# Kernel optimization log

Hardware: AMD Instinct MI355X
Metric: run time of the kernel (lower is better)

Reference implementation:

```python
import jax, jax.numpy as jnp
import numpy as np

B, N, E, I, H = 8, 20000, 320000, 32, 64


def setup_inputs() -> dict:
    key = jax.random.key(0)
    ks = jax.random.split(key, 12)
    s = 0.05
    return {
        "x": jax.random.normal(ks[0], (B, I), jnp.float32),
        "h_prev": jax.random.normal(ks[1], (B, N, H), jnp.float32),
        "src": jax.random.randint(ks[2], (E,), 0, N, jnp.int32),
        "dst": jax.random.randint(ks[3], (E,), 0, N, jnp.int32),
        "w_r_w": jax.random.normal(ks[4], (I, H), jnp.float32) * s,
        "w_r_b": jnp.zeros((H,), jnp.float32),
        "w_z_w": jax.random.normal(ks[5], (I, H), jnp.float32) * s,
        "w_z_b": jnp.zeros((H,), jnp.float32),
        "w_h_w": jax.random.normal(ks[6], (I, H), jnp.float32) * s,
        "w_h_b": jnp.zeros((H,), jnp.float32),
        "gcn_w": jax.random.normal(ks[7], (H, H), jnp.float32) * s,
        "gcn_b": jnp.zeros((H,), jnp.float32),
    }


def _graph_conv(h, src, dst, gcn_w, gcn_b):
    # DGL GraphConv, norm='both': rst = D_in^{-1/2} A (D_out^{-1/2} (H W)) + b
    num_nodes = h.shape[1]
    ones = jnp.ones((src.shape[0],), h.dtype)
    out_deg = jax.ops.segment_sum(ones, src, num_segments=num_nodes)
    in_deg = jax.ops.segment_sum(ones, dst, num_segments=num_nodes)
    out_norm = jax.lax.rsqrt(jnp.clip(out_deg, 1.0))  # [N]
    in_norm = jax.lax.rsqrt(jnp.clip(in_deg, 1.0))    # [N]
    hw = jnp.einsum('bnh,hk->nbk', h, gcn_w)           # [N,B,H] node-major
    feat = hw * out_norm[:, None, None]
    msgs = feat[src]                                   # [E,B,H] gather
    agg = jax.ops.segment_sum(msgs, dst, num_segments=num_nodes)  # [N,B,H]
    agg = agg * in_norm[:, None, None]
    return jnp.swapaxes(agg, 0, 1) + gcn_b             # [B,N,H]


def reference(x, h_prev, src, dst, w_r_w, w_r_b, w_z_w, w_z_b, w_h_w, w_h_b,
              gcn_w, gcn_b):
    # gcn_h is the same module applied to the same h_prev three times in the
    # original -> compute the aggregation once (identical math).
    a = _graph_conv(h_prev, src, dst, gcn_w, gcn_b)    # [B,N,H]
    xr = (x @ w_r_w + w_r_b)[:, None, :]               # [B,1,H] broadcast over nodes
    xz = (x @ w_z_w + w_z_b)[:, None, :]
    xh = (x @ w_h_w + w_h_b)[:, None, :]
    r_t = jax.nn.sigmoid(xr + a)
    z_t = jax.nn.sigmoid(xz + a)
    h_tilde = jnp.tanh(xh + r_t * a)
    h_t = (1.0 - z_t) * h_prev + z_t * h_tilde
    return h_t
```

## Files before the change

kernel.cpp:

```cpp
#include <hip/hip_runtime.h>
#include <hip/hip_bf16.h>
#include <cstdint>

constexpr int B = 8;
constexpr int N = 20000;
constexpr int E = 320000;
constexpr int I = 32;
constexpr int H = 64;
constexpr int BH = B * H;
constexpr int CAP = 64;

constexpr int GCN_BLOCKS  = 625;
constexpr int SCAT_BLOCKS = E / 256;

typedef short short8 __attribute__((ext_vector_type(8)));
typedef float f32x4 __attribute__((ext_vector_type(4)));
typedef float f32x2 __attribute__((ext_vector_type(2)));

__device__ __forceinline__ float bf2f(unsigned short u) {
    union { unsigned int i; float f; } c;
    c.i = ((unsigned int)u) << 16;
    return c.f;
}
__device__ __forceinline__ unsigned short f2bf(float f) {
    unsigned int u = __float_as_uint(f);
    u += 0x7fffu + ((u >> 16) & 1u);
    return (unsigned short)(u >> 16);
}
__device__ __forceinline__ float sigmoidf_(float v) {
    return 1.f / (1.f + __expf(-v));
}
__device__ __forceinline__ float tanhf_(float v) {
    return 2.f / (1.f + __expf(-2.f * v)) - 1.f;
}

__global__ __launch_bounds__(256) void fused_pre(
    const float* __restrict__ h_prev, const float* __restrict__ gcn_w,
    const int* __restrict__ src, const int* __restrict__ dst,
    int* __restrict__ cursor, int* __restrict__ out_cnt,
    unsigned short* __restrict__ slots,
    const float* __restrict__ x,
    const float* __restrict__ wr, const float* __restrict__ br,
    const float* __restrict__ wz, const float* __restrict__ bz,
    const float* __restrict__ wh, const float* __restrict__ bh,
    float* __restrict__ xrzh,
    unsigned char* __restrict__ feat)
{
    __shared__ __attribute__((aligned(16))) unsigned short Wt[64 * 72];
    __shared__ __attribute__((aligned(16))) char tbuf[4][1024];
    __shared__ float xs[B * I];

    int bid = blockIdx.x;
    int tid = threadIdx.x;

    if (bid >= GCN_BLOCKS) {
        if (bid < GCN_BLOCKS + SCAT_BLOCKS) {
            int i = (bid - GCN_BLOCKS) * 256 + tid;
            int s = src[i];
            int d = dst[i];
            int pos = atomicAdd(&cursor[d], 1);
            if (pos < CAP) slots[d * CAP + pos] = (unsigned short)s;
            atomicAdd(&out_cnt[s], 1);
        } else {
            xs[tid] = x[tid];
            __syncthreads();
            for (int idx = tid; idx < 3 * BH; idx += 256) {
                int mat = idx >> 9;
                int rem = idx & 511;
                int b   = rem >> 6;
                int k   = rem & 63;
                const float* w    = (mat == 0) ? wr : (mat == 1) ? wz : wh;
                const float* bias = (mat == 0) ? br : (mat == 1) ? bz : bh;
                float acc = bias[k];
                #pragma unroll
                for (int i = 0; i < I; ++i)
                    acc = fmaf(xs[b * I + i], w[i * H + k], acc);
                xrzh[idx] = acc;
            }
        }
        return;
    }

    int w    = tid >> 6;
    int lane = tid & 63;
    int r = lane & 15;
    int g = lane >> 4;

    for (int i2 = tid; i2 < H * H; i2 += 256) {
        int hh = i2 >> 6, kk = i2 & 63;
        Wt[kk * 72 + hh] = f2bf(gcn_w[i2]);
    }
    __syncthreads();

    short8 bfrag[2][4];
    #pragma unroll
    for (int kt = 0; kt < 2; ++kt)
        #pragma unroll
        for (int nt = 0; nt < 4; ++nt)
            bfrag[kt][nt] = *(const short8*)&Wt[(nt * 16 + r) * 72 + kt * 32 + g * 8];

    int b = r & 7;
    char* tb8 = tbuf[w];
    int wv = bid * 4 + w;
    for (int np = wv; np < N / 2; np += 4 * GCN_BLOCKS) {
        int node = 2 * np + (r >> 3);
        const float* hp = h_prev + ((size_t)b * N + node) * H + g * 8;
        f32x4 x0 = __builtin_nontemporal_load((const f32x4*)hp);
        f32x4 x1 = __builtin_nontemporal_load((const f32x4*)(hp + 4));
        f32x4 x2 = __builtin_nontemporal_load((const f32x4*)(hp + 32));
        f32x4 x3 = __builtin_nontemporal_load((const f32x4*)(hp + 36));
        short8 a0, a1;
        #pragma unroll
        for (int j = 0; j < 4; ++j) {
            a0[j]     = (short)f2bf(x0[j]);
            a0[j + 4] = (short)f2bf(x1[j]);
            a1[j]     = (short)f2bf(x2[j]);
            a1[j + 4] = (short)f2bf(x3[j]);
        }
        f32x4 acc[4];
        #pragma unroll
        for (int nt = 0; nt < 4; ++nt) { acc[nt][0] = 0.f; acc[nt][1] = 0.f; acc[nt][2] = 0.f; acc[nt][3] = 0.f; }
        #pragma unroll
        for (int nt = 0; nt < 4; ++nt)
            acc[nt] = __builtin_amdgcn_mfma_f32_16x16x32_bf16(a0, bfrag[0][nt], acc[nt], 0, 0, 0);
        #pragma unroll
        for (int nt = 0; nt < 4; ++nt)
            acc[nt] = __builtin_amdgcn_mfma_f32_16x16x32_bf16(a1, bfrag[1][nt], acc[nt], 0, 0, 0);

        #pragma unroll
        for (int nt = 0; nt < 4; ++nt) {
            int v = __builtin_amdgcn_cvt_pk_fp8_f32(acc[nt][0], acc[nt][1], 0, false);
            v = __builtin_amdgcn_cvt_pk_fp8_f32(acc[nt][2], acc[nt][3], v, true);
            int ob = (g >> 1) * 512 + (nt * 16 + r) * 8 + (g & 1) * 4;
            *(int*)&tb8[ob] = v;
        }
        int4 vv = *(const int4*)(tb8 + lane * 16);
        *(int4*)(feat + (size_t)np * 1024 + lane * 16) = vv;
    }
}

__global__ __launch_bounds__(256) void agg_gru(
    const unsigned char* __restrict__ feat,
    const int* __restrict__ in_cnt,
    const int* __restrict__ out_cnt,
    const unsigned short* __restrict__ slots,
    const float* __restrict__ xrzh,
    const float* __restrict__ gcn_b,
    const float* __restrict__ h_prev,
    float* __restrict__ out)
{
    int n    = blockIdx.x * 4 + (threadIdx.x >> 6);
    n = __builtin_amdgcn_readfirstlane(n);
    int lane = threadIdx.x & 63;

    int cnt_raw = in_cnt[n];
    int cnt = min(cnt_raw, CAP);
    int my_sv = 0;
    if (lane < cnt) {
        int s = (int)__builtin_nontemporal_load(slots + (size_t)n * CAP + lane);
        float on = rsqrtf(fmaxf((float)out_cnt[s], 1.f));
        my_sv = ((int)f2bf(on) << 16) | s;
    }

    float acc[8] = {0.f, 0.f, 0.f, 0.f, 0.f, 0.f, 0.f, 0.f};
    int i = 0;
    for (; i + 4 <= cnt; i += 4) {
        #pragma unroll
        for (int u = 0; u < 4; ++u) {
            int sv = __builtin_amdgcn_readlane(my_sv, i + u);
            const uint2* row = (const uint2*)(feat + (sv & 0xffff) * 512);
            uint2 v = row[lane];
            float o = __uint_as_float((unsigned)sv & 0xffff0000u);
            f32x2 p01 = __builtin_amdgcn_cvt_pk_f32_fp8((int)v.x, false);
            f32x2 p23 = __builtin_amdgcn_cvt_pk_f32_fp8((int)v.x, true);
            f32x2 p45 = __builtin_amdgcn_cvt_pk_f32_fp8((int)v.y, false);
            f32x2 p67 = __builtin_amdgcn_cvt_pk_f32_fp8((int)v.y, true);
            acc[0] = fmaf(o, p01[0], acc[0]); acc[1] = fmaf(o, p01[1], acc[1]);
            acc[2] = fmaf(o, p23[0], acc[2]); acc[3] = fmaf(o, p23[1], acc[3]);
            acc[4] = fmaf(o, p45[0], acc[4]); acc[5] = fmaf(o, p45[1], acc[5]);
            acc[6] = fmaf(o, p67[0], acc[6]); acc[7] = fmaf(o, p67[1], acc[7]);
        }
    }
    for (; i < cnt; ++i) {
        int sv = __builtin_amdgcn_readlane(my_sv, i);
        const uint2* row = (const uint2*)(feat + (sv & 0xffff) * 512);
        uint2 v = row[lane];
        float o = __uint_as_float((unsigned)sv & 0xffff0000u);
        f32x2 p01 = __builtin_amdgcn_cvt_pk_f32_fp8((int)v.x, false);
        f32x2 p23 = __builtin_amdgcn_cvt_pk_f32_fp8((int)v.x, true);
        f32x2 p45 = __builtin_amdgcn_cvt_pk_f32_fp8((int)v.y, false);
        f32x2 p67 = __builtin_amdgcn_cvt_pk_f32_fp8((int)v.y, true);
        acc[0] = fmaf(o, p01[0], acc[0]); acc[1] = fmaf(o, p01[1], acc[1]);
        acc[2] = fmaf(o, p23[0], acc[2]); acc[3] = fmaf(o, p23[1], acc[3]);
        acc[4] = fmaf(o, p45[0], acc[4]); acc[5] = fmaf(o, p45[1], acc[5]);
        acc[6] = fmaf(o, p67[0], acc[6]); acc[7] = fmaf(o, p67[1], acc[7]);
    }

    float innorm = rsqrtf(fmaxf((float)cnt_raw, 1.f));
    float gb = gcn_b[lane];
    #pragma unroll
    for (int b = 0; b < 8; ++b) {
        float a  = fmaf(acc[b], innorm, gb);
        float xr = xrzh[b * H + lane];
        float xz = xrzh[BH + b * H + lane];
        float xh = xrzh[2 * BH + b * H + lane];
        float rr = sigmoidf_(xr + a);
        float zz = sigmoidf_(xz + a);
        float tt = tanhf_(xh + rr * a);
        size_t hidx = ((size_t)b * N + n) * H + lane;
        float hp = __builtin_nontemporal_load(h_prev + hidx);
        __builtin_nontemporal_store((1.f - zz) * hp + zz * tt, out + hidx);
    }
}

extern "C" void kernel_launch(void* const* d_in, const int* in_sizes, int n_in,
                              void* d_out, int out_size, void* d_ws, size_t ws_size,
                              hipStream_t stream) {
    const float* x      = (const float*)d_in[0];
    const float* h_prev = (const float*)d_in[1];
    const int*   src    = (const int*)d_in[2];
    const int*   dst    = (const int*)d_in[3];
    const float* w_r_w  = (const float*)d_in[4];
    const float* w_r_b  = (const float*)d_in[5];
    const float* w_z_w  = (const float*)d_in[6];
    const float* w_z_b  = (const float*)d_in[7];
    const float* w_h_w  = (const float*)d_in[8];
    const float* w_h_b  = (const float*)d_in[9];
    const float* gcn_w  = (const float*)d_in[10];
    const float* gcn_b  = (const float*)d_in[11];
    float* out = (float*)d_out;

    char* ws = (char*)d_ws;
    size_t off = 0;
    unsigned char* feat = (unsigned char*)(ws + off); off += (size_t)N * BH;
    off = (off + 255) & ~(size_t)255;
    float* xrzh = (float*)(ws + off);  off += (size_t)3 * BH * sizeof(float);
    off = (off + 255) & ~(size_t)255;
    int* cnts = (int*)(ws + off);
    int* cursor  = cnts;
    int* out_cnt = cnts + N;           off += (size_t)2 * N * sizeof(int);
    unsigned short* slots = (unsigned short*)(ws + off);
    off += (size_t)N * CAP * sizeof(unsigned short);

    hipMemsetAsync(cnts, 0, (size_t)2 * N * sizeof(int), stream);

    fused_pre<<<GCN_BLOCKS + SCAT_BLOCKS + 1, 256, 0, stream>>>(
        h_prev, gcn_w, src, dst, cursor, out_cnt, slots,
        x, w_r_w, w_r_b, w_z_w, w_z_b, w_h_w, w_h_b, xrzh, feat);

    agg_gru<<<N / 4, 256, 0, stream>>>(
        feat, cursor, out_cnt, slots, xrzh, gcn_b, h_prev, out);
}
```

Before: 81.46 us.

## Merge memset, preprocessing and aggregation into one cooperative persistent kernel

Replaces the memset plus two kernel launches with a single cooperative kernel of 1024 persistent blocks. Grid-wide syncs separate counter zeroing, the GEMM/scatter phase and the aggregation/GRU phase, and each block runs grid-stride loops over its share of work. This removes launch gaps and lets the separate phases share the GPU, but fewer GCN blocks and grid.sync overhead may cut parallelism. It also drops the nontemporal loads and pads the neighbor loop to a multiple of four.

```diff
diff --git a/kernel.cpp b/kernel.cpp
--- a/kernel.cpp
+++ b/kernel.cpp
@@ -1,6 +1,8 @@
 #include <hip/hip_runtime.h>
-#include <hip/hip_bf16.h>
+#include <hip/hip_cooperative_groups.h>
 #include <cstdint>
+
+namespace cg = cooperative_groups;
 
 constexpr int B = 8;
 constexpr int N = 20000;
@@ -10,18 +12,13 @@
 constexpr int BH = B * H;
 constexpr int CAP = 64;
 
-constexpr int GCN_BLOCKS  = 625;
-constexpr int SCAT_BLOCKS = E / 256;
+constexpr int NBLK    = 1024;
+constexpr int GCN_BLK = 256;
 
 typedef short short8 __attribute__((ext_vector_type(8)));
 typedef float f32x4 __attribute__((ext_vector_type(4)));
 typedef float f32x2 __attribute__((ext_vector_type(2)));
 
-__device__ __forceinline__ float bf2f(unsigned short u) {
-    union { unsigned int i; float f; } c;
-    c.i = ((unsigned int)u) << 16;
-    return c.f;
-}
 __device__ __forceinline__ unsigned short f2bf(float f) {
     unsigned int u = __float_as_uint(f);
     u += 0x7fffu + ((u >> 16) & 1u);
@@ -34,7 +31,7 @@
     return 2.f / (1.f + __expf(-2.f * v)) - 1.f;
 }
 
-__global__ __launch_bounds__(256) void fused_pre(
+__device__ __forceinline__ void do_pre(int nblk,
     const float* __restrict__ h_prev, const float* __restrict__ gcn_w,
     const int* __restrict__ src, const int* __restrict__ dst,
     int* __restrict__ cursor, int* __restrict__ out_cnt,
@@ -48,98 +45,94 @@
 {
     __shared__ __attribute__((aligned(16))) unsigned short Wt[64 * 72];
     __shared__ __attribute__((aligned(16))) char tbuf[4][1024];
-    __shared__ float xs[B * I];
-
     int bid = blockIdx.x;
     int tid = threadIdx.x;
-
-    if (bid >= GCN_BLOCKS) {
-        if (bid < GCN_BLOCKS + SCAT_BLOCKS) {
-            int i = (bid - GCN_BLOCKS) * 256 + tid;
-            int s = src[i];
-            int d = dst[i];
+    int w    = tid >> 6;
+    int lane = tid & 63;
+
+    if (bid < GCN_BLK) {
+        int r = lane & 15;
+        int g = lane >> 4;
+        for (int i2 = tid; i2 < H * H; i2 += 256) {
+            int hh = i2 >> 6, kk = i2 & 63;
+            Wt[kk * 72 + hh] = f2bf(gcn_w[i2]);
+        }
+        __syncthreads();
+        short8 bfrag[2][4];
+        #pragma unroll
+        for (int kt = 0; kt < 2; ++kt)
+            #pragma unroll
+            for (int nt = 0; nt < 4; ++nt)
+                bfrag[kt][nt] = *(const short8*)&Wt[(nt * 16 + r) * 72 + kt * 32 + g * 8];
+
+        int b = r & 7;
+        char* tb8 = tbuf[w];
+        int wv = bid * 4 + w;
+        for (int np = wv; np < N / 2; np += 4 * GCN_BLK) {
+            int node = 2 * np + (r >> 3);
+            const float* hp = h_prev + ((size_t)b * N + node) * H + g * 8;
+            f32x4 x0 = *(const f32x4*)hp;
+            f32x4 x1 = *(const f32x4*)(hp + 4);
+            f32x4 x2 = *(const f32x4*)(hp + 32);
+            f32x4 x3 = *(const f32x4*)(hp + 36);
+            short8 a0, a1;
+            #pragma unroll
+            for (int j = 0; j < 4; ++j) {
+                a0[j]     = (short)f2bf(x0[j]);
+                a0[j + 4] = (short)f2bf(x1[j]);
+                a1[j]     = (short)f2bf(x2[j]);
+                a1[j + 4] = (short)f2bf(x3[j]);
+            }
+            f32x4 acc[4];
+            #pragma unroll
+            for (int nt = 0; nt < 4; ++nt) { acc[nt][0] = 0.f; acc[nt][1] = 0.f; acc[nt][2] = 0.f; acc[nt][3] = 0.f; }
+            #pragma unroll
+            for (int nt = 0; nt < 4; ++nt)
+                acc[nt] = __builtin_amdgcn_mfma_f32_16x16x32_bf16(a0, bfrag[0][nt], acc[nt], 0, 0, 0);
+            #pragma unroll
+            for (int nt = 0; nt < 4; ++nt)
+                acc[nt] = __builtin_amdgcn_mfma_f32_16x16x32_bf16(a1, bfrag[1][nt], acc[nt], 0, 0, 0);
+
+            #pragma unroll
+            for (int nt = 0; nt < 4; ++nt) {
+                int v = __builtin_amdgcn_cvt_pk_fp8_f32(acc[nt][0], acc[nt][1], 0, false);
+                v = __builtin_amdgcn_cvt_pk_fp8_f32(acc[nt][2], acc[nt][3], v, true);
+                int ob = (g >> 1) * 512 + (nt * 16 + r) * 8 + (g & 1) * 4;
+                *(int*)&tb8[ob] = v;
+            }
+            int4 vv = *(const int4*)(tb8 + lane * 16);
+            *(int4*)(feat + (size_t)np * 1024 + lane * 16) = vv;
+        }
+    } else if (bid < nblk - 1) {
+        int nscat = nblk - 1 - GCN_BLK;
+        for (int e = (bid - GCN_BLK) * 256 + tid; e < E; e += nscat * 256) {
+            int s = src[e];
+            int d = dst[e];
             int pos = atomicAdd(&cursor[d], 1);
             if (pos < CAP) slots[d * CAP + pos] = (unsigned short)s;
             atomicAdd(&out_cnt[s], 1);
-        } else {
-            xs[tid] = x[tid];
-            __syncthreads();
-            for (int idx = tid; idx < 3 * BH; idx += 256) {
-                int mat = idx >> 9;
-                int rem = idx & 511;
-                int b   = rem >> 6;
-                int k   = rem & 63;
-                const float* w    = (mat == 0) ? wr : (mat == 1) ? wz : wh;
-                const float* bias = (mat == 0) ? br : (mat == 1) ? bz : bh;
-                float acc = bias[k];
-                #pragma unroll
-                for (int i = 0; i < I; ++i)
-                    acc = fmaf(xs[b * I + i], w[i * H + k], acc);
-                xrzh[idx] = acc;
-            }
-        }
-        return;
+        }
+    } else {
+        __shared__ float xs[B * I];
+        xs[tid] = x[tid];
+        __syncthreads();
+        for (int idx = tid; idx < 3 * BH; idx += 256) {
+            int mat = idx >> 9;
+            int rem = idx & 511;
+            int b   = rem >> 6;
+            int k   = rem & 63;
+            const float* wm   = (mat == 0) ? wr : (mat == 1) ? wz : wh;
+            const float* bias = (mat == 0) ? br : (mat == 1) ? bz : bh;
+            float acc = bias[k];
+            #pragma unroll
+            for (int i = 0; i < I; ++i)
+                acc = fmaf(xs[b * I + i], wm[i * H + k], acc);
+            xrzh[idx] = acc;
+        }
     }
-
-    int w    = tid >> 6;
-    int lane = tid & 63;
-    int r = lane & 15;
-    int g = lane >> 4;
-
-    for (int i2 = tid; i2 < H * H; i2 += 256) {
-        int hh = i2 >> 6, kk = i2 & 63;
-        Wt[kk * 72 + hh] = f2bf(gcn_w[i2]);
-    }
-    __syncthreads();
-
-    short8 bfrag[2][4];
-    #pragma unroll
-    for (int kt = 0; kt < 2; ++kt)
-        #pragma unroll
-        for (int nt = 0; nt < 4; ++nt)
-            bfrag[kt][nt] = *(const short8*)&Wt[(nt * 16 + r) * 72 + kt * 32 + g * 8];
-
-    int b = r & 7;
-    char* tb8 = tbuf[w];
-    int wv = bid * 4 + w;
-    for (int np = wv; np < N / 2; np += 4 * GCN_BLOCKS) {
-        int node = 2 * np + (r >> 3);
-        const float* hp = h_prev + ((size_t)b * N + node) * H + g * 8;
-        f32x4 x0 = __builtin_nontemporal_load((const f32x4*)hp);
-        f32x4 x1 = __builtin_nontemporal_load((const f32x4*)(hp + 4));
-        f32x4 x2 = __builtin_nontemporal_load((const f32x4*)(hp + 32));
-        f32x4 x3 = __builtin_nontemporal_load((const f32x4*)(hp + 36));
-        short8 a0, a1;
-        #pragma unroll
-        for (int j = 0; j < 4; ++j) {
-            a0[j]     = (short)f2bf(x0[j]);
-            a0[j + 4] = (short)f2bf(x1[j]);
-            a1[j]     = (short)f2bf(x2[j]);
-            a1[j + 4] = (short)f2bf(x3[j]);
-        }
-        f32x4 acc[4];
-        #pragma unroll
-        for (int nt = 0; nt < 4; ++nt) { acc[nt][0] = 0.f; acc[nt][1] = 0.f; acc[nt][2] = 0.f; acc[nt][3] = 0.f; }
-        #pragma unroll
-        for (int nt = 0; nt < 4; ++nt)
-            acc[nt] = __builtin_amdgcn_mfma_f32_16x16x32_bf16(a0, bfrag[0][nt], acc[nt], 0, 0, 0);
-        #pragma unroll
-        for (int nt = 0; nt < 4; ++nt)
-            acc[nt] = __builtin_amdgcn_mfma_f32_16x16x32_bf16(a1, bfrag[1][nt], acc[nt], 0, 0, 0);
-
-        #pragma unroll
-        for (int nt = 0; nt < 4; ++nt) {
-            int v = __builtin_amdgcn_cvt_pk_fp8_f32(acc[nt][0], acc[nt][1], 0, false);
-            v = __builtin_amdgcn_cvt_pk_fp8_f32(acc[nt][2], acc[nt][3], v, true);
-            int ob = (g >> 1) * 512 + (nt * 16 + r) * 8 + (g & 1) * 4;
-            *(int*)&tb8[ob] = v;
-        }
-        int4 vv = *(const int4*)(tb8 + lane * 16);
-        *(int4*)(feat + (size_t)np * 1024 + lane * 16) = vv;
-    }
-}
-
-__global__ __launch_bounds__(256) void agg_gru(
+}
+
+__device__ __forceinline__ void do_agg(int nblk,
     const unsigned char* __restrict__ feat,
     const int* __restrict__ in_cnt,
     const int* __restrict__ out_cnt,
@@ -149,68 +142,109 @@
     const float* __restrict__ h_prev,
     float* __restrict__ out)
 {
-    int n    = blockIdx.x * 4 + (threadIdx.x >> 6);
-    n = __builtin_amdgcn_readfirstlane(n);
-    int lane = threadIdx.x & 63;
-
-    int cnt_raw = in_cnt[n];
-    int cnt = min(cnt_raw, CAP);
-    int my_sv = 0;
-    if (lane < cnt) {
-        int s = (int)__builtin_nontemporal_load(slots + (size_t)n * CAP + lane);
-        float on = rsqrtf(fmaxf((float)out_cnt[s], 1.f));
-        my_sv = ((int)f2bf(on) << 16) | s;
+    int tid  = threadIdx.x;
+    int w    = tid >> 6;
+    int lane = tid & 63;
+    for (int n0 = blockIdx.x * 4 + w; n0 < N; n0 += nblk * 4) {
+        int n = __builtin_amdgcn_readfirstlane(n0);
+        int cnt_raw = in_cnt[n];
+        int cnt = min(cnt_raw, CAP);
+        int my_sv = 0;
+        if (lane < cnt) {
+            int s = (int)slots[(size_t)n * CAP + lane];
+            float on = rsqrtf(fmaxf((float)out_cnt[s], 1.f));
+            my_sv = ((int)f2bf(on) << 16) | s;
+        }
+        int ru = (cnt + 3) & ~3;
+
+        f32x2 acc01 = {0.f, 0.f}, acc23 = {0.f, 0.f};
+        f32x2 acc45 = {0.f, 0.f}, acc67 = {0.f, 0.f};
+        for (int i = 0; i < ru; i += 4) {
+            #pragma unroll
+            for (int u = 0; u < 4; ++u) {
+                int sv = __builtin_amdgcn_readlane(my_sv, i + u);
+                const uint2* row = (const uint2*)(feat + (size_t)((unsigned)sv & 0xffffu) * 512);
+                uint2 v = row[lane];
+                float o = __uint_as_float((unsigned)sv & 0xffff0000u);
+                f32x2 o2 = {o, o};
+                acc01 += o2 * __builtin_amdgcn_cvt_pk_f32_fp8((int)v.x, false);
+                acc23 += o2 * __builtin_amdgcn_cvt_pk_f32_fp8((int)v.x, true);
+                acc45 += o2 * __builtin_amdgcn_cvt_pk_f32_fp8((int)v.y, false);
+                acc67 += o2 * __builtin_amdgcn_cvt_pk_f32_fp8((int)v.y, true);
+            }
+        }
+        float acc[8] = {acc01[0], acc01[1], acc23[0], acc23[1],
+                        acc45[0], acc45[1], acc67[0], acc67[1]};
+
+        float innorm = rsqrtf(fmaxf((float)cnt_raw, 1.f));
+        float gb = gcn_b[lane];
+        #pragma unroll
+        for (int b = 0; b < 8; ++b) {
+            float a  = fmaf(acc[b], innorm, gb);
+            float xr = xrzh[b * H + lane];
+            float xz = xrzh[BH + b * H + lane];
+            float xh = xrzh[2 * BH + b * H + lane];
+            float rr = sigmoidf_(xr + a);
+            float zz = sigmoidf_(xz + a);
+            float tt = tanhf_(xh + rr * a);
+            size_t hidx = ((size_t)b * N + n) * H + lane;
+            float hp = h_prev[hidx];
+            __builtin_nontemporal_store((1.f - zz) * hp + zz * tt, out + hidx);
+        }
     }
-
-    float acc[8] = {0.f, 0.f, 0.f, 0.f, 0.f, 0.f, 0.f, 0.f};
-    int i = 0;
-    for (; i + 4 <= cnt; i += 4) {
-        #pragma unroll
-        for (int u = 0; u < 4; ++u) {
-            int sv = __builtin_amdgcn_readlane(my_sv, i + u);
-            const uint2* row = (const uint2*)(feat + (sv & 0xffff) * 512);
-            uint2 v = row[lane];
-            float o = __uint_as_float((unsigned)sv & 0xffff0000u);
-            f32x2 p01 = __builtin_amdgcn_cvt_pk_f32_fp8((int)v.x, false);
-            f32x2 p23 = __builtin_amdgcn_cvt_pk_f32_fp8((int)v.x, true);
-            f32x2 p45 = __builtin_amdgcn_cvt_pk_f32_fp8((int)v.y, false);
-            f32x2 p67 = __builtin_amdgcn_cvt_pk_f32_fp8((int)v.y, true);
-            acc[0] = fmaf(o, p01[0], acc[0]); acc[1] = fmaf(o, p01[1], acc[1]);
-            acc[2] = fmaf(o, p23[0], acc[2]); acc[3] = fmaf(o, p23[1], acc[3]);
-            acc[4] = fmaf(o, p45[0], acc[4]); acc[5] = fmaf(o, p45[1], acc[5]);
-            acc[6] = fmaf(o, p67[0], acc[6]); acc[7] = fmaf(o, p67[1], acc[7]);
-        }
-    }
-    for (; i < cnt; ++i) {
-        int sv = __builtin_amdgcn_readlane(my_sv, i);
-        const uint2* row = (const uint2*)(feat + (sv & 0xffff) * 512);
-        uint2 v = row[lane];
-        float o = __uint_as_float((unsigned)sv & 0xffff0000u);
-        f32x2 p01 = __builtin_amdgcn_cvt_pk_f32_fp8((int)v.x, false);
-        f32x2 p23 = __builtin_amdgcn_cvt_pk_f32_fp8((int)v.x, true);
-        f32x2 p45 = __builtin_amdgcn_cvt_pk_f32_fp8((int)v.y, false);
-        f32x2 p67 = __builtin_amdgcn_cvt_pk_f32_fp8((int)v.y, true);
-        acc[0] = fmaf(o, p01[0], acc[0]); acc[1] = fmaf(o, p01[1], acc[1]);
-        acc[2] = fmaf(o, p23[0], acc[2]); acc[3] = fmaf(o, p23[1], acc[3]);
-        acc[4] = fmaf(o, p45[0], acc[4]); acc[5] = fmaf(o, p45[1], acc[5]);
-        acc[6] = fmaf(o, p67[0], acc[6]); acc[7] = fmaf(o, p67[1], acc[7]);
-    }
-
-    float innorm = rsqrtf(fmaxf((float)cnt_raw, 1.f));
-    float gb = gcn_b[lane];
-    #pragma unroll
-    for (int b = 0; b < 8; ++b) {
-        float a  = fmaf(acc[b], innorm, gb);
-        float xr = xrzh[b * H + lane];
-        float xz = xrzh[BH + b * H + lane];
-        float xh = xrzh[2 * BH + b * H + lane];
-        float rr = sigmoidf_(xr + a);
-        float zz = sigmoidf_(xz + a);
-        float tt = tanhf_(xh + rr * a);
-        size_t hidx = ((size_t)b * N + n) * H + lane;
-        float hp = __builtin_nontemporal_load(h_prev + hidx);
-        __builtin_nontemporal_store((1.f - zz) * hp + zz * tt, out + hidx);
-    }
+}
+
+__global__ __launch_bounds__(256, 4) void mono(
+    const float* __restrict__ h_prev, const float* __restrict__ gcn_w,
+    const int* __restrict__ src, const int* __restrict__ dst,
+    int* __restrict__ cursor, int* __restrict__ out_cnt,
+    unsigned short* __restrict__ slots,
+    const float* __restrict__ x,
+    const float* __restrict__ wr, const float* __restrict__ br,
+    const float* __restrict__ wz, const float* __restrict__ bz,
+    const float* __restrict__ wh, const float* __restrict__ bh,
+    float* __restrict__ xrzh,
+    unsigned char* __restrict__ feat,
+    const float* __restrict__ gcn_b,
+    float* __restrict__ out)
+{
+    cg::grid_group grid = cg::this_grid();
+    for (int i = blockIdx.x * 256 + threadIdx.x; i < 2 * N; i += NBLK * 256)
+        cursor[i] = 0;
+    grid.sync();
+    do_pre(NBLK, h_prev, gcn_w, src, dst, cursor, out_cnt, slots,
+           x, wr, br, wz, bz, wh, bh, xrzh, feat);
+    grid.sync();
+    do_agg(NBLK, feat, cursor, out_cnt, slots, xrzh, gcn_b, h_prev, out);
+}
+
+__global__ __launch_bounds__(256) void pre_k(
+    const float* __restrict__ h_prev, const float* __restrict__ gcn_w,
+    const int* __restrict__ src, const int* __restrict__ dst,
+    int* __restrict__ cursor, int* __restrict__ out_cnt,
+    unsigned short* __restrict__ slots,
+    const float* __restrict__ x,
+    const float* __restrict__ wr, const float* __restrict__ br,
+    const float* __restrict__ wz, const float* __restrict__ bz,
+    const float* __restrict__ wh, const float* __restrict__ bh,
+    float* __restrict__ xrzh,
+    unsigned char* __restrict__ feat)
+{
+    do_pre(gridDim.x, h_prev, gcn_w, src, dst, cursor, out_cnt, slots,
+           x, wr, br, wz, bz, wh, bh, xrzh, feat);
+}
+
+__global__ __launch_bounds__(256) void agg_k(
+    const unsigned char* __restrict__ feat,
+    const int* __restrict__ in_cnt,
+    const int* __restrict__ out_cnt,
+    const unsigned short* __restrict__ slots,
+    const float* __restrict__ xrzh,
+    const float* __restrict__ gcn_b,
+    const float* __restrict__ h_prev,
+    float* __restrict__ out)
+{
+    do_agg(gridDim.x, feat, in_cnt, out_cnt, slots, xrzh, gcn_b, h_prev, out);
 }
 
 extern "C" void kernel_launch(void* const* d_in, const int* in_sizes, int n_in,
@@ -242,12 +276,22 @@
     unsigned short* slots = (unsigned short*)(ws + off);
     off += (size_t)N * CAP * sizeof(unsigned short);
 
-    hipMemsetAsync(cnts, 0, (size_t)2 * N * sizeof(int), stream);
-
-    fused_pre<<<GCN_BLOCKS + SCAT_BLOCKS + 1, 256, 0, stream>>>(
-        h_prev, gcn_w, src, dst, cursor, out_cnt, slots,
-        x, w_r_w, w_r_b, w_z_w, w_z_b, w_h_w, w_h_b, xrzh, feat);
-
-    agg_gru<<<N / 4, 256, 0, stream>>>(
-        feat, cursor, out_cnt, slots, xrzh, gcn_b, h_prev, out);
-}
+    void* args[] = {
+        (void*)&h_prev, (void*)&gcn_w, (void*)&src, (void*)&dst,
+        (void*)&cursor, (void*)&out_cnt, (void*)&slots,
+        (void*)&x, (void*)&w_r_w, (void*)&w_r_b, (void*)&w_z_w, (void*)&w_z_b,
+        (void*)&w_h_w, (void*)&w_h_b, (void*)&xrzh, (void*)&feat,
+        (void*)&gcn_b, (void*)&out
+    };
+    hipError_t err = hipLaunchCooperativeKernel((const void*)mono, dim3(NBLK),
+                                                dim3(256), args, 0, stream);
+    if (err != hipSuccess) {
+        (void)hipGetLastError();
+        hipMemsetAsync(cnts, 0, (size_t)2 * N * sizeof(int), stream);
+        pre_k<<<NBLK, 256, 0, stream>>>(h_prev, gcn_w, src, dst, cursor, out_cnt,
+                                        slots, x, w_r_w, w_r_b, w_z_w, w_z_b,
+                                        w_h_w, w_h_b, xrzh, feat);
+        agg_k<<<N / 4, 256, 0, stream>>>(feat, cursor, out_cnt, slots, xrzh,
+                                         gcn_b, h_prev, out);
+    }
+}
```

After: 245.3 us. 3.01x slower.
